# Kernel optimization log

Measured on AMD Instinct MI355X. Metric: run time of the kernel, lower is better.

The kernel has to match this reference:

```python
import jax, jax.numpy as jnp
import numpy as np

KERNEL = 3  # 2*half_size + 1 with half_size=1
ITER = 20


def _pool(v):
    # MaxPool2d(kernel=3, stride=1, padding=1) == SAME max reduce_window on NCHW
    return jax.lax.reduce_window(v, -jnp.inf, jax.lax.max,
                                 (1, 1, KERNEL, KERNEL), (1, 1, 1, 1), 'SAME')


def _erode(v):
    return -_pool(-v)


def setup_inputs() -> dict:
    key = jax.random.key(0)
    x = jax.random.normal(key, (16, 1, 1024, 1024), dtype=jnp.float32)
    return {"x": x}


def reference(x):
    skel0 = x - _pool(_erode(x))  # open(x) = dilate(erode(x))

    def step(carry, _):
        xc, skel = carry
        xc = _erode(xc)
        skel = skel + (xc - _pool(_erode(xc)))
        return (xc, skel), None

    (_, skel), _ = jax.lax.scan(step, (x, skel0), None, length=ITER)
    return skel
```

## Files before the change

### kernel.cpp

```cpp
#include <hip/hip_runtime.h>


static constexpr int W = 1024, H = 1024, NIMG = 16;
static constexpr int RCH = 32;
static constexpr int WPB = 2;
static constexpr int NBAND = 9;
static constexpr float BIG = 3.0e38f;

__device__ __forceinline__ float min3f(float a, float b, float c) { return fminf(fminf(a, b), c); }
__device__ __forceinline__ float max3f(float a, float b, float c) { return fmaxf(fmaxf(a, b), c); }

__device__ __forceinline__ float dpp_left(float v) {
    return __int_as_float(__builtin_amdgcn_mov_dpp(__float_as_int(v), 0x138, 0xF, 0xF, true));
}
__device__ __forceinline__ float dpp_right(float v) {
    return __int_as_float(__builtin_amdgcn_mov_dpp(__float_as_int(v), 0x130, 0xF, 0xF, true));
}

template<bool FIRST, bool WRITE_E, bool EDGE, bool LE, bool RE, int MODE>
__device__ __forceinline__
void pipe_step2(int t, int y0, int gx,
                bool leftEdge, bool rightEdge, bool lane_ok,
                const float* __restrict__ in, float* __restrict__ eo,
                float* __restrict__ sk,
                float2 (&OB)[7], float2 (&MB)[7], float2& OD, float2& MD,
                float2 (&acc)[8], float2 (&pf)[2])
{
    float2 cur0, cur1;
    if (!EDGE || (unsigned)t < (unsigned)H)       cur0 = pf[0];
    else                                          cur0 = make_float2(BIG, BIG);
    if (!EDGE || (unsigned)(t + 1) < (unsigned)H) cur1 = pf[1];
    else                                          cur1 = make_float2(BIG, BIG);
    {
        const int n0 = t + 2, n1 = t + 3;
        if (MODE != 1 || ((!EDGE || (unsigned)n0 < (unsigned)H) && n0 <= y0 + RCH + 7))
            pf[0] = *(const float2*)&in[(size_t)n0 * W + gx];
        if (MODE != 1 || ((!EDGE || (unsigned)n1 < (unsigned)H) && n1 <= y0 + RCH + 7))
            pf[1] = *(const float2*)&in[(size_t)n1 * W + gx];
    }

#pragma unroll
    for (int s = 0; s < 7; ++s) {
        const float2 fOld = OB[s];
        const float2 fMid = MB[s];

        float2 vm0, vm1;
        vm0.x = min3f(fOld.x, fMid.x, cur0.x);
        vm0.y = min3f(fOld.y, fMid.y, cur0.y);
        vm1.x = min3f(fMid.x, cur0.x, cur1.x);
        vm1.y = min3f(fMid.y, cur0.y, cur1.y);
        float l0 = dpp_left(vm0.y), r0 = dpp_right(vm0.x);
        float l1 = dpp_left(vm1.y), r1 = dpp_right(vm1.x);
        if (LE && leftEdge)  { l0 = BIG; l1 = BIG; }
        if (RE && rightEdge) { r0 = BIG; r1 = BIG; }
        float2 en0, en1;
        en0.x = min3f(l0,    vm0.x, vm0.y);
        en0.y = min3f(vm0.x, vm0.y, r0);
        en1.x = min3f(l1,    vm1.x, vm1.y);
        en1.y = min3f(vm1.x, vm1.y, r1);

        if (MODE != 0) {
            float2 gOld, gMid;
            if (s < 6) { gOld = OB[s + 1]; gMid = MB[s + 1]; }
            else       { gOld = OD;        gMid = MD;        }
            float2 vx0, vx1;
            if (!EDGE) {
                vx0.x = max3f(gOld.x, gMid.x, en0.x);
                vx0.y = max3f(gOld.y, gMid.y, en0.y);
                vx1.x = max3f(gMid.x, en0.x, en1.x);
                vx1.y = max3f(gMid.y, en0.y, en1.y);
            } else {
                const bool topOK0 = (t - s - 3) >= 0, botOK0 = (t - s - 1) < H;
                const bool topOK1 = (t - s - 2) >= 0, botOK1 = (t - s) < H;
                vx0.x = max3f(topOK0 ? gOld.x : -BIG, gMid.x, botOK0 ? en0.x : -BIG);
                vx0.y = max3f(topOK0 ? gOld.y : -BIG, gMid.y, botOK0 ? en0.y : -BIG);
                vx1.x = max3f(topOK1 ? gMid.x : -BIG, en0.x, botOK1 ? en1.x : -BIG);
                vx1.y = max3f(topOK1 ? gMid.y : -BIG, en0.y, botOK1 ? en1.y : -BIG);
            }
            float dl0 = dpp_left(vx0.y), dr0 = dpp_right(vx0.x);
            float dl1 = dpp_left(vx1.y), dr1 = dpp_right(vx1.x);
            if (LE && leftEdge)  { dl0 = -BIG; dl1 = -BIG; }
            if (RE && rightEdge) { dr0 = -BIG; dr1 = -BIG; }
            float2 dn0, dn1;
            dn0.x = max3f(dl0,   vx0.x, vx0.y);
            dn0.y = max3f(vx0.x, vx0.y, dr0);
            dn1.x = max3f(dl1,   vx1.x, vx1.y);
            dn1.y = max3f(vx1.x, vx1.y, dr1);

            if (FIRST && s == 0) {
                acc[6].x = fOld.x - dn0.x;  acc[6].y = fOld.y - dn0.y;
                acc[7].x = fMid.x - dn1.x;  acc[7].y = fMid.y - dn1.y;
            } else {
                acc[6 - s].x += fOld.x - dn0.x;  acc[6 - s].y += fOld.y - dn0.y;
                acc[7 - s].x += fMid.x - dn1.x;  acc[7 - s].y += fMid.y - dn1.y;
            }
        }

        OB[s] = cur0;
        MB[s] = cur1;

        if (s == 6) {
            if (WRITE_E && MODE != 0) {
                const int er0 = t - 7, er1 = t - 6;
                if (MODE == 2) {
                    if (lane_ok) {
                        *(float2*)&eo[(size_t)er0 * W + gx] = en0;
                        *(float2*)&eo[(size_t)er1 * W + gx] = en1;
                    }
                } else {
                    if (er0 >= y0 && er0 < y0 + RCH && lane_ok)
                        *(float2*)&eo[(size_t)er0 * W + gx] = en0;
                    if (er1 >= y0 && er1 < y0 + RCH && lane_ok)
                        *(float2*)&eo[(size_t)er1 * W + gx] = en1;
                }
            }
            OD = en0;
            MD = en1;
        }
        cur0 = en0;
        cur1 = en1;
    }

    if (MODE != 0) {
        if (MODE == 2) {
            if (lane_ok) {
                *(float2*)&sk[(size_t)(t - 8) * W + gx] = acc[0];
                *(float2*)&sk[(size_t)(t - 7) * W + gx] = acc[1];
            }
        } else {
            if (t >= y0 + 8 && lane_ok) {
                *(float2*)&sk[(size_t)(t - 8) * W + gx] = acc[0];
                *(float2*)&sk[(size_t)(t - 7) * W + gx] = acc[1];
            }
        }
#pragma unroll
        for (int j = 0; j < 6; ++j) acc[j] = acc[j + 2];
        if (!FIRST) {
            if (MODE == 2) {
                acc[6] = *(const float2*)&sk[(size_t)t * W + gx];
                acc[7] = *(const float2*)&sk[(size_t)(t + 1) * W + gx];
            } else {
                if (t >= y0 && t < y0 + RCH)
                    acc[6] = *(const float2*)&sk[(size_t)t * W + gx];
                if (t + 1 >= y0 && t + 1 < y0 + RCH)
                    acc[7] = *(const float2*)&sk[(size_t)(t + 1) * W + gx];
            }
        }
    }
}

template<bool FIRST, bool WRITE_E, bool LE, bool RE>
__device__ __forceinline__
void sweep_int(int y0, int gx, bool leftEdge, bool rightEdge, bool lane_ok,
               const float* __restrict__ in, float* __restrict__ eo,
               float* __restrict__ sk)
{
    float2 OB[7], MB[7], OD, MD, acc[8], pf[2];
    const float2 big2 = make_float2(BIG, BIG);
    const float2 z2   = make_float2(0.f, 0.f);
#pragma unroll
    for (int s = 0; s < 7; ++s) { OB[s] = big2; MB[s] = big2; }
    OD = big2; MD = big2;
#pragma unroll
    for (int j = 0; j < 8; ++j) acc[j] = z2;
    pf[0] = *(const float2*)&in[(size_t)(y0 - 8) * W + gx];
    pf[1] = *(const float2*)&in[(size_t)(y0 - 7) * W + gx];

    int t = y0 - 8;
#pragma unroll
    for (int i = 0; i < 4; ++i, t += 2)
        pipe_step2<FIRST, WRITE_E, false, LE, RE, 0>(t, y0, gx, leftEdge, rightEdge, lane_ok,
                                                     in, eo, sk, OB, MB, OD, MD, acc, pf);
#pragma unroll 1
    for (int i = 0; i < 4; ++i, t += 2)
        pipe_step2<FIRST, WRITE_E, false, LE, RE, 1>(t, y0, gx, leftEdge, rightEdge, lane_ok,
                                                     in, eo, sk, OB, MB, OD, MD, acc, pf);
#pragma unroll 1
    for (int i = 0; i < 12; ++i, t += 2)
        pipe_step2<FIRST, WRITE_E, false, LE, RE, 2>(t, y0, gx, leftEdge, rightEdge, lane_ok,
                                                     in, eo, sk, OB, MB, OD, MD, acc, pf);
#pragma unroll 1
    for (int i = 0; i < 4; ++i, t += 2)
        pipe_step2<FIRST, WRITE_E, false, LE, RE, 1>(t, y0, gx, leftEdge, rightEdge, lane_ok,
                                                     in, eo, sk, OB, MB, OD, MD, acc, pf);
}

template<bool FIRST, bool WRITE_E, bool LE, bool RE>
__device__ __forceinline__
void sweep_edge(int y0, int gx, bool leftEdge, bool rightEdge, bool lane_ok,
                const float* __restrict__ in, float* __restrict__ eo,
                float* __restrict__ sk)
{
    float2 OB[7], MB[7], OD, MD, acc[8], pf[2];
    const float2 big2 = make_float2(BIG, BIG);
    const float2 z2   = make_float2(0.f, 0.f);
#pragma unroll
    for (int s = 0; s < 7; ++s) { OB[s] = big2; MB[s] = big2; }
    OD = big2; MD = big2;
#pragma unroll
    for (int j = 0; j < 8; ++j) acc[j] = z2;
    pf[0] = big2; pf[1] = big2;
    {
        const int r0 = y0 - 8, r1 = y0 - 7;
        if (r0 >= 0) pf[0] = *(const float2*)&in[(size_t)r0 * W + gx];
        if (r1 >= 0) pf[1] = *(const float2*)&in[(size_t)r1 * W + gx];
    }

    int t = y0 - 8;
#pragma unroll 1
    for (int i = 0; i < (RCH + 16) / 2; ++i, t += 2)
        pipe_step2<FIRST, WRITE_E, true, LE, RE, 1>(t, y0, gx, leftEdge, rightEdge, lane_ok,
                                                    in, eo, sk, OB, MB, OD, MD, acc, pf);
}

template<bool FIRST, bool WRITE_E>
__global__ __launch_bounds__(WPB * 64)
void skel_pipe(const float* __restrict__ ein, float* __restrict__ eout,
               float* __restrict__ skel)
{
    const int lane = threadIdx.x;
    const int bx = blockIdx.x;
    const int y0 = (blockIdx.y * WPB + (int)threadIdx.y) * RCH;
    const int img = blockIdx.z;
    const int x0 = (bx == 0) ? 0 : ((bx == NBAND - 1) ? (W - 128) : 112 * bx);
    const int gx = x0 + 2 * lane;

    const size_t base = (size_t)img * (size_t)(W * H);
    const float* __restrict__ in = ein + base;
    float* __restrict__ eo = eout + base;
    float* __restrict__ sk = skel + base;

    const bool leftEdge  = (gx == 0);
    const bool rightEdge = (gx + 2 == W);
    const int own_lo = (bx == 0) ? 0 : 112 * bx + 8;
    const int own_hi = (bx == NBAND - 1) ? W : 112 * (bx + 1) + 8;
    const bool lane_ok = (gx >= own_lo) && (gx < own_hi);

    const bool interior = (y0 >= 32 && y0 <= H - RCH - 32);

    if (bx == 0) {
        if (interior) sweep_int <FIRST, WRITE_E, true,  false>(y0, gx, leftEdge, rightEdge, lane_ok, in, eo, sk);
        else          sweep_edge<FIRST, WRITE_E, true,  false>(y0, gx, leftEdge, rightEdge, lane_ok, in, eo, sk);
    } else if (bx == NBAND - 1) {
        if (interior) sweep_int <FIRST, WRITE_E, false, true >(y0, gx, leftEdge, rightEdge, lane_ok, in, eo, sk);
        else          sweep_edge<FIRST, WRITE_E, false, true >(y0, gx, leftEdge, rightEdge, lane_ok, in, eo, sk);
    } else {
        if (interior) sweep_int <FIRST, WRITE_E, false, false>(y0, gx, leftEdge, rightEdge, lane_ok, in, eo, sk);
        else          sweep_edge<FIRST, WRITE_E, false, false>(y0, gx, leftEdge, rightEdge, lane_ok, in, eo, sk);
    }
}

extern "C" void kernel_launch(void* const* d_in, const int* in_sizes, int n_in,
                              void* d_out, int out_size, void* d_ws, size_t ws_size,
                              hipStream_t stream)
{
    const float* x = (const float*)d_in[0];
    float* skel = (float*)d_out;
    const size_t n = (size_t)NIMG * W * H;

    float* e0 = (float*)d_ws;
    float* e1 = e0 + n;

    dim3 grid(NBAND, H / (RCH * WPB), NIMG);
    dim3 block(64, WPB);

    skel_pipe<true,  true ><<<grid, block, 0, stream>>>(x,  e0, skel);
    skel_pipe<false, true ><<<grid, block, 0, stream>>>(e0, e1, skel);
    skel_pipe<false, false><<<grid, block, 0, stream>>>(e1, e0, skel);
}
```

Measured before the change: 302.9 us.

## Generalize pipeline depth and fuse iterations into two deeper kernel passes

Templates the per-thread erosion pipeline depth so one pass can fuse 10 or 11 erosion stages instead of 7, letting the 21 stages run in two launches instead of three. Row chunks grow to 64 and column bands change to 10 with a 12-pixel halo, which keeps redundant halo work manageable at the greater depth. This removes one full read and write of the intermediate image and one skeleton read-modify-write pass. In exchange each thread holds more pipeline registers, which may lower occupancy, and there are fewer row blocks to spread across the GPU.

New measurement: 312.5 us. 1.03x slower.

```diff
diff --git a/kernel.cpp b/kernel.cpp
--- a/kernel.cpp
+++ b/kernel.cpp
@@ -2,9 +2,9 @@
 
 
 static constexpr int W = 1024, H = 1024, NIMG = 16;
-static constexpr int RCH = 32;
+static constexpr int RCH = 64;
 static constexpr int WPB = 2;
-static constexpr int NBAND = 9;
+static constexpr int NBAND = 10;
 static constexpr float BIG = 3.0e38f;
 
 __device__ __forceinline__ float min3f(float a, float b, float c) { return fminf(fminf(a, b), c); }
@@ -17,14 +17,14 @@
     return __int_as_float(__builtin_amdgcn_mov_dpp(__float_as_int(v), 0x130, 0xF, 0xF, true));
 }
 
-template<bool FIRST, bool WRITE_E, bool EDGE, bool LE, bool RE, int MODE>
+template<int G, bool FIRST, bool WRITE_E, bool EDGE, bool LE, bool RE, int MODE>
 __device__ __forceinline__
 void pipe_step2(int t, int y0, int gx,
                 bool leftEdge, bool rightEdge, bool lane_ok,
                 const float* __restrict__ in, float* __restrict__ eo,
                 float* __restrict__ sk,
-                float2 (&OB)[7], float2 (&MB)[7], float2& OD, float2& MD,
-                float2 (&acc)[8], float2 (&pf)[2])
+                float2 (&OB)[G], float2 (&MB)[G], float2& OD, float2& MD,
+                float2 (&acc)[G + 3], float2 (&pf)[2])
 {
     float2 cur0, cur1;
     if (!EDGE || (unsigned)t < (unsigned)H)       cur0 = pf[0];
@@ -33,14 +33,14 @@
     else                                          cur1 = make_float2(BIG, BIG);
     {
         const int n0 = t + 2, n1 = t + 3;
-        if (MODE != 1 || ((!EDGE || (unsigned)n0 < (unsigned)H) && n0 <= y0 + RCH + 7))
+        if (MODE != 1 || ((!EDGE || (unsigned)n0 < (unsigned)H) && n0 <= y0 + RCH + G))
             pf[0] = *(const float2*)&in[(size_t)n0 * W + gx];
-        if (MODE != 1 || ((!EDGE || (unsigned)n1 < (unsigned)H) && n1 <= y0 + RCH + 7))
+        if (MODE != 1 || ((!EDGE || (unsigned)n1 < (unsigned)H) && n1 <= y0 + RCH + G))
             pf[1] = *(const float2*)&in[(size_t)n1 * W + gx];
     }
 
 #pragma unroll
-    for (int s = 0; s < 7; ++s) {
+    for (int s = 0; s < G; ++s) {
         const float2 fOld = OB[s];
         const float2 fMid = MB[s];
 
@@ -61,8 +61,8 @@
 
         if (MODE != 0) {
             float2 gOld, gMid;
-            if (s < 6) { gOld = OB[s + 1]; gMid = MB[s + 1]; }
-            else       { gOld = OD;        gMid = MD;        }
+            if (s < G - 1) { gOld = OB[s + 1]; gMid = MB[s + 1]; }
+            else           { gOld = OD;        gMid = MD;        }
             float2 vx0, vx1;
             if (!EDGE) {
                 vx0.x = max3f(gOld.x, gMid.x, en0.x);
@@ -88,20 +88,20 @@
             dn1.y = max3f(vx1.x, vx1.y, dr1);
 
             if (FIRST && s == 0) {
-                acc[6].x = fOld.x - dn0.x;  acc[6].y = fOld.y - dn0.y;
-                acc[7].x = fMid.x - dn1.x;  acc[7].y = fMid.y - dn1.y;
+                acc[G - 1].x = fOld.x - dn0.x;  acc[G - 1].y = fOld.y - dn0.y;
+                acc[G].x     = fMid.x - dn1.x;  acc[G].y     = fMid.y - dn1.y;
             } else {
-                acc[6 - s].x += fOld.x - dn0.x;  acc[6 - s].y += fOld.y - dn0.y;
-                acc[7 - s].x += fMid.x - dn1.x;  acc[7 - s].y += fMid.y - dn1.y;
+                acc[G - 1 - s].x += fOld.x - dn0.x;  acc[G - 1 - s].y += fOld.y - dn0.y;
+                acc[G - s].x     += fMid.x - dn1.x;  acc[G - s].y     += fMid.y - dn1.y;
             }
         }
 
         OB[s] = cur0;
         MB[s] = cur1;
 
-        if (s == 6) {
+        if (s == G - 1) {
             if (WRITE_E && MODE != 0) {
-                const int er0 = t - 7, er1 = t - 6;
+                const int er0 = t - G, er1 = t - G + 1;
                 if (MODE == 2) {
                     if (lane_ok) {
                         *(float2*)&eo[(size_t)er0 * W + gx] = en0;
@@ -124,96 +124,103 @@
     if (MODE != 0) {
         if (MODE == 2) {
             if (lane_ok) {
-                *(float2*)&sk[(size_t)(t - 8) * W + gx] = acc[0];
-                *(float2*)&sk[(size_t)(t - 7) * W + gx] = acc[1];
+                *(float2*)&sk[(size_t)(t - (G + 1)) * W + gx] = acc[0];
+                *(float2*)&sk[(size_t)(t - G) * W + gx]       = acc[1];
             }
         } else {
-            if (t >= y0 + 8 && lane_ok) {
-                *(float2*)&sk[(size_t)(t - 8) * W + gx] = acc[0];
-                *(float2*)&sk[(size_t)(t - 7) * W + gx] = acc[1];
-            }
-        }
-#pragma unroll
-        for (int j = 0; j < 6; ++j) acc[j] = acc[j + 2];
+            if (t >= y0 + G + 1 && lane_ok) {
+                *(float2*)&sk[(size_t)(t - (G + 1)) * W + gx] = acc[0];
+                *(float2*)&sk[(size_t)(t - G) * W + gx]       = acc[1];
+            }
+        }
+#pragma unroll
+        for (int j = 0; j <= G; ++j) acc[j] = acc[j + 2];
         if (!FIRST) {
             if (MODE == 2) {
-                acc[6] = *(const float2*)&sk[(size_t)t * W + gx];
-                acc[7] = *(const float2*)&sk[(size_t)(t + 1) * W + gx];
+                acc[G + 1] = *(const float2*)&sk[(size_t)(t + 2) * W + gx];
+                acc[G + 2] = *(const float2*)&sk[(size_t)(t + 3) * W + gx];
             } else {
-                if (t >= y0 && t < y0 + RCH)
-                    acc[6] = *(const float2*)&sk[(size_t)t * W + gx];
-                if (t + 1 >= y0 && t + 1 < y0 + RCH)
-                    acc[7] = *(const float2*)&sk[(size_t)(t + 1) * W + gx];
-            }
-        }
-    }
-}
-
-template<bool FIRST, bool WRITE_E, bool LE, bool RE>
+                if (t + 2 >= y0 && t + 2 < y0 + RCH)
+                    acc[G + 1] = *(const float2*)&sk[(size_t)(t + 2) * W + gx];
+                if (t + 3 >= y0 && t + 3 < y0 + RCH)
+                    acc[G + 2] = *(const float2*)&sk[(size_t)(t + 3) * W + gx];
+            }
+        }
+    }
+}
+
+template<int G, bool FIRST, bool WRITE_E, bool LE, bool RE>
 __device__ __forceinline__
 void sweep_int(int y0, int gx, bool leftEdge, bool rightEdge, bool lane_ok,
                const float* __restrict__ in, float* __restrict__ eo,
                float* __restrict__ sk)
 {
-    float2 OB[7], MB[7], OD, MD, acc[8], pf[2];
+    float2 OB[G], MB[G], OD, MD, acc[G + 3], pf[2];
     const float2 big2 = make_float2(BIG, BIG);
     const float2 z2   = make_float2(0.f, 0.f);
 #pragma unroll
-    for (int s = 0; s < 7; ++s) { OB[s] = big2; MB[s] = big2; }
+    for (int s = 0; s < G; ++s) { OB[s] = big2; MB[s] = big2; }
     OD = big2; MD = big2;
 #pragma unroll
-    for (int j = 0; j < 8; ++j) acc[j] = z2;
-    pf[0] = *(const float2*)&in[(size_t)(y0 - 8) * W + gx];
-    pf[1] = *(const float2*)&in[(size_t)(y0 - 7) * W + gx];
-
-    int t = y0 - 8;
-#pragma unroll
-    for (int i = 0; i < 4; ++i, t += 2)
-        pipe_step2<FIRST, WRITE_E, false, LE, RE, 0>(t, y0, gx, leftEdge, rightEdge, lane_ok,
-                                                     in, eo, sk, OB, MB, OD, MD, acc, pf);
-#pragma unroll 1
-    for (int i = 0; i < 4; ++i, t += 2)
-        pipe_step2<FIRST, WRITE_E, false, LE, RE, 1>(t, y0, gx, leftEdge, rightEdge, lane_ok,
-                                                     in, eo, sk, OB, MB, OD, MD, acc, pf);
-#pragma unroll 1
-    for (int i = 0; i < 12; ++i, t += 2)
-        pipe_step2<FIRST, WRITE_E, false, LE, RE, 2>(t, y0, gx, leftEdge, rightEdge, lane_ok,
-                                                     in, eo, sk, OB, MB, OD, MD, acc, pf);
-#pragma unroll 1
-    for (int i = 0; i < 4; ++i, t += 2)
-        pipe_step2<FIRST, WRITE_E, false, LE, RE, 1>(t, y0, gx, leftEdge, rightEdge, lane_ok,
-                                                     in, eo, sk, OB, MB, OD, MD, acc, pf);
-}
-
-template<bool FIRST, bool WRITE_E, bool LE, bool RE>
+    for (int j = 0; j < G + 3; ++j) acc[j] = z2;
+    pf[0] = *(const float2*)&in[(size_t)(y0 - (G + 1)) * W + gx];
+    pf[1] = *(const float2*)&in[(size_t)(y0 - G) * W + gx];
+
+    constexpr int TOTAL  = RCH / 2 + G + 1;
+    constexpr int WARM   = (G - 1 - ((G + 1) & 1)) / 2;
+    constexpr int GUARDN = (G + 3 + ((G + 1) & 1)) / 2;
+    constexpr int STEADY = TOTAL - WARM - 2 * GUARDN;
+    static_assert(STEADY > 0, "phase layout");
+
+    int t = y0 - (G + 1);
+#pragma unroll
+    for (int i = 0; i < WARM; ++i, t += 2)
+        pipe_step2<G, FIRST, WRITE_E, false, LE, RE, 0>(t, y0, gx, leftEdge, rightEdge, lane_ok,
+                                                        in, eo, sk, OB, MB, OD, MD, acc, pf);
+#pragma unroll 1
+    for (int i = 0; i < GUARDN; ++i, t += 2)
+        pipe_step2<G, FIRST, WRITE_E, false, LE, RE, 1>(t, y0, gx, leftEdge, rightEdge, lane_ok,
+                                                        in, eo, sk, OB, MB, OD, MD, acc, pf);
+#pragma unroll 1
+    for (int i = 0; i < STEADY; ++i, t += 2)
+        pipe_step2<G, FIRST, WRITE_E, false, LE, RE, 2>(t, y0, gx, leftEdge, rightEdge, lane_ok,
+                                                        in, eo, sk, OB, MB, OD, MD, acc, pf);
+#pragma unroll 1
+    for (int i = 0; i < GUARDN; ++i, t += 2)
+        pipe_step2<G, FIRST, WRITE_E, false, LE, RE, 1>(t, y0, gx, leftEdge, rightEdge, lane_ok,
+                                                        in, eo, sk, OB, MB, OD, MD, acc, pf);
+}
+
+template<int G, bool FIRST, bool WRITE_E, bool LE, bool RE>
 __device__ __forceinline__
 void sweep_edge(int y0, int gx, bool leftEdge, bool rightEdge, bool lane_ok,
                 const float* __restrict__ in, float* __restrict__ eo,
                 float* __restrict__ sk)
 {
-    float2 OB[7], MB[7], OD, MD, acc[8], pf[2];
+    float2 OB[G], MB[G], OD, MD, acc[G + 3], pf[2];
     const float2 big2 = make_float2(BIG, BIG);
     const float2 z2   = make_float2(0.f, 0.f);
 #pragma unroll
-    for (int s = 0; s < 7; ++s) { OB[s] = big2; MB[s] = big2; }
+    for (int s = 0; s < G; ++s) { OB[s] = big2; MB[s] = big2; }
     OD = big2; MD = big2;
 #pragma unroll
-    for (int j = 0; j < 8; ++j) acc[j] = z2;
+    for (int j = 0; j < G + 3; ++j) acc[j] = z2;
     pf[0] = big2; pf[1] = big2;
     {
-        const int r0 = y0 - 8, r1 = y0 - 7;
+        const int r0 = y0 - (G + 1), r1 = y0 - G;
         if (r0 >= 0) pf[0] = *(const float2*)&in[(size_t)r0 * W + gx];
         if (r1 >= 0) pf[1] = *(const float2*)&in[(size_t)r1 * W + gx];
     }
 
-    int t = y0 - 8;
-#pragma unroll 1
-    for (int i = 0; i < (RCH + 16) / 2; ++i, t += 2)
-        pipe_step2<FIRST, WRITE_E, true, LE, RE, 1>(t, y0, gx, leftEdge, rightEdge, lane_ok,
-                                                    in, eo, sk, OB, MB, OD, MD, acc, pf);
-}
-
-template<bool FIRST, bool WRITE_E>
+    constexpr int TOTAL = RCH / 2 + G + 1;
+    int t = y0 - (G + 1);
+#pragma unroll 1
+    for (int i = 0; i < TOTAL; ++i, t += 2)
+        pipe_step2<G, FIRST, WRITE_E, true, LE, RE, 1>(t, y0, gx, leftEdge, rightEdge, lane_ok,
+                                                       in, eo, sk, OB, MB, OD, MD, acc, pf);
+}
+
+template<int G, bool FIRST, bool WRITE_E>
 __global__ __launch_bounds__(WPB * 64)
 void skel_pipe(const float* __restrict__ ein, float* __restrict__ eout,
                float* __restrict__ skel)
@@ -222,7 +229,7 @@
     const int bx = blockIdx.x;
     const int y0 = (blockIdx.y * WPB + (int)threadIdx.y) * RCH;
     const int img = blockIdx.z;
-    const int x0 = (bx == 0) ? 0 : ((bx == NBAND - 1) ? (W - 128) : 112 * bx);
+    const int x0 = (bx == 0) ? 0 : ((bx == NBAND - 1) ? (W - 128) : 100 * bx);
     const int gx = x0 + 2 * lane;
 
     const size_t base = (size_t)img * (size_t)(W * H);
@@ -232,21 +239,21 @@
 
     const bool leftEdge  = (gx == 0);
     const bool rightEdge = (gx + 2 == W);
-    const int own_lo = (bx == 0) ? 0 : 112 * bx + 8;
-    const int own_hi = (bx == NBAND - 1) ? W : 112 * (bx + 1) + 8;
+    const int own_lo = (bx == 0) ? 0 : 100 * bx + 12;
+    const int own_hi = (bx == NBAND - 1) ? W : 100 * bx + 112;
     const bool lane_ok = (gx >= own_lo) && (gx < own_hi);
 
-    const bool interior = (y0 >= 32 && y0 <= H - RCH - 32);
+    const bool interior = (y0 >= 64 && y0 <= H - RCH - 64);
 
     if (bx == 0) {
-        if (interior) sweep_int <FIRST, WRITE_E, true,  false>(y0, gx, leftEdge, rightEdge, lane_ok, in, eo, sk);
-        else          sweep_edge<FIRST, WRITE_E, true,  false>(y0, gx, leftEdge, rightEdge, lane_ok, in, eo, sk);
+        if (interior) sweep_int <G, FIRST, WRITE_E, true,  false>(y0, gx, leftEdge, rightEdge, lane_ok, in, eo, sk);
+        else          sweep_edge<G, FIRST, WRITE_E, true,  false>(y0, gx, leftEdge, rightEdge, lane_ok, in, eo, sk);
     } else if (bx == NBAND - 1) {
-        if (interior) sweep_int <FIRST, WRITE_E, false, true >(y0, gx, leftEdge, rightEdge, lane_ok, in, eo, sk);
-        else          sweep_edge<FIRST, WRITE_E, false, true >(y0, gx, leftEdge, rightEdge, lane_ok, in, eo, sk);
+        if (interior) sweep_int <G, FIRST, WRITE_E, false, true >(y0, gx, leftEdge, rightEdge, lane_ok, in, eo, sk);
+        else          sweep_edge<G, FIRST, WRITE_E, false, true >(y0, gx, leftEdge, rightEdge, lane_ok, in, eo, sk);
     } else {
-        if (interior) sweep_int <FIRST, WRITE_E, false, false>(y0, gx, leftEdge, rightEdge, lane_ok, in, eo, sk);
-        else          sweep_edge<FIRST, WRITE_E, false, false>(y0, gx, leftEdge, rightEdge, lane_ok, in, eo, sk);
+        if (interior) sweep_int <G, FIRST, WRITE_E, false, false>(y0, gx, leftEdge, rightEdge, lane_ok, in, eo, sk);
+        else          sweep_edge<G, FIRST, WRITE_E, false, false>(y0, gx, leftEdge, rightEdge, lane_ok, in, eo, sk);
     }
 }
 
@@ -256,15 +263,12 @@
 {
     const float* x = (const float*)d_in[0];
     float* skel = (float*)d_out;
-    const size_t n = (size_t)NIMG * W * H;
-
-    float* e0 = (float*)d_ws;
-    float* e1 = e0 + n;
+
+    float* e10 = (float*)d_ws;
 
     dim3 grid(NBAND, H / (RCH * WPB), NIMG);
     dim3 block(64, WPB);
 
-    skel_pipe<true,  true ><<<grid, block, 0, stream>>>(x,  e0, skel);
-    skel_pipe<false, true ><<<grid, block, 0, stream>>>(e0, e1, skel);
-    skel_pipe<false, false><<<grid, block, 0, stream>>>(e1, e0, skel);
-}
+    skel_pipe<10, true,  true ><<<grid, block, 0, stream>>>(x,   e10, skel);
+    skel_pipe<11, false, false><<<grid, block, 0, stream>>>(e10, e10, skel);
+}
```
